# Kernel optimization log

Measured on AMD Instinct MI355X. Metric: run time of the kernel, lower is better.

## Reference

```python
import jax, jax.numpy as jnp
import numpy as np

D = 16        # d_model
DFF = 128     # ffn hidden
H_NN = 128    # pairwise-MLP hidden
RES = 1.0     # res_ratio (undefined global in source; standard residual)
EPS = 1e-6


def setup_inputs() -> dict:
    key = jax.random.key(0)
    ks = jax.random.split(key, 16)
    B, G, L = 8, 1, 256
    def n(k, shape, s=0.05):
        return jax.random.normal(k, shape, jnp.float32) * s
    return dict(
        x=jax.random.normal(ks[0], (B, G, L, D), jnp.float32),
        mask=jnp.zeros((B, G, L, L), jnp.float32),
        wq=n(ks[1], (D, D)), bq=jnp.zeros((D,), jnp.float32),
        wk=n(ks[2], (D, D)), bk=jnp.zeros((D,), jnp.float32),
        wv=n(ks[3], (D, D)), bv=jnp.zeros((D,), jnp.float32),
        wo=n(ks[4], (D, D)), bo=jnp.zeros((D,), jnp.float32),
        nn_w1=n(ks[5], (2 * D, H_NN)), nn_b1=jnp.zeros((H_NN,), jnp.float32),
        nn_w2=n(ks[6], (H_NN, 1)), nn_b2=jnp.zeros((1,), jnp.float32),
        f1=n(ks[7], (D, DFF)), f1b=jnp.zeros((DFF,), jnp.float32),
        f2=n(ks[8], (DFF, D)), f2b=jnp.zeros((D,), jnp.float32),
        g1=jnp.ones((D,), jnp.float32), be1=jnp.zeros((D,), jnp.float32),
        g2=jnp.ones((D,), jnp.float32), be2=jnp.zeros((D,), jnp.float32),
    )


def _layernorm(x, g, b):
    m = jnp.mean(x, -1, keepdims=True)
    v = jnp.var(x, -1, keepdims=True)
    return (x - m) * jax.lax.rsqrt(v + EPS) * g + b


def reference(x, mask, wq, bq, wk, bk, wv, bv, wo, bo,
              nn_w1, nn_b1, nn_w2, nn_b2,
              f1, f1b, f2, f2b, g1, be1, g2, be2):
    # projections: (B,G,L,D)
    q = x @ wq + bq
    k = x @ wk + bk
    v = x @ wv + bv
    # pairwise relation-network attention.
    # NN(concat([q_i, k_j])) first layer splits as q_i @ W1[:D] + k_j @ W1[D:]
    w1q, w1k = nn_w1[:D], nn_w1[D:]
    w2 = nn_w2[:, 0]
    qa = q @ w1q  # (B,G,L,H)
    kb = k @ w1k
    h1 = jax.nn.relu(qa[:, :, :, None, :] + kb[:, :, None, :, :] + nn_b1)  # (B,G,Lq,Lk,H)
    logits = jnp.einsum('bgijh,h->bgij', h1, w2) + nn_b2[0]
    # make_sym: NN(concat([k_j, q_i])) -> k_j @ W1[:D] + q_i @ W1[D:]
    ka = k @ w1q
    qb = q @ w1k
    h2 = jax.nn.relu(qb[:, :, :, None, :] + ka[:, :, None, :, :] + nn_b1)
    logits = logits + jnp.einsum('bgijh,h->bgij', h2, w2) + nn_b2[0]
    logits = logits + mask * -1e9
    attn = jax.nn.softmax(logits, axis=-1)          # (B,G,Lq,Lk)
    ctx = jnp.einsum('bgij,bgjd->bgid', attn, v)    # (B,G,L,D)
    attn_out = ctx @ wo + bo
    out1 = _layernorm(RES * x + (2.0 - RES) * attn_out, g1, be1)
    ffn = jax.nn.relu(out1 @ f1 + f1b) @ f2 + f2b
    out2 = _layernorm(RES * out1 + (2.0 - RES) * ffn, g2, be2)
    return out2
```

## Files before the change

### kernel.cpp

```cpp
#include <hip/hip_runtime.h>
#include <hip/hip_bf16.h>

typedef __hip_bfloat16 bf16;
typedef float f32x4 __attribute__((ext_vector_type(4)));

constexpr int DIM  = 16;
constexpr int HNN  = 128;
constexpr int SEQ  = 256;
constexpr int BAT  = 8;
constexpr int ROWS = BAT * SEQ;
constexpr int HP   = HNN / 2;
constexpr int QT   = 4;
constexpr int NQT  = ROWS / QT;
constexpr int QHP  = 16;

__device__ __forceinline__ bool is_f32(const void* g1) {
  return ((const unsigned*)g1)[0] == 0x3F800000u;
}
__device__ __forceinline__ float ld(const void* p, long i, bool f32) {
  return f32 ? ((const float*)p)[i]
             : __bfloat162float(((const bf16*)p)[i]);
}

__global__ __launch_bounds__(128) void prep_kernel(
    const void* __restrict__ x,
    const void* __restrict__ wq, const void* __restrict__ bq,
    const void* __restrict__ wk, const void* __restrict__ bk,
    const void* __restrict__ wv, const void* __restrict__ bv,
    const void* __restrict__ nn_w1, const void* __restrict__ nn_b1,
    const void* __restrict__ nn_w2, const void* __restrict__ g1flag,
    float* __restrict__ kkT, float* __restrict__ qq,
    float* __restrict__ vT,  float2* __restrict__ w2p)
{
  const bool f32 = is_f32(g1flag);
  const int row = blockIdx.x;
  const int tid = threadIdx.x;
  __shared__ float xs[DIM], qs[DIM], ks[DIM], vs[DIM];

  if (tid < DIM) xs[tid] = ld(x, (long)row * DIM + tid, f32);
  __syncthreads();

  if (tid < 3 * DIM) {
    const int which = tid >> 4, d = tid & 15;
    const void* w  = (which == 0) ? wq : (which == 1) ? wk : wv;
    const void* bb = (which == 0) ? bq : (which == 1) ? bk : bv;
    float acc = ld(bb, d, f32);
    #pragma unroll
    for (int e = 0; e < DIM; e++) acc += xs[e] * ld(w, e * DIM + d, f32);
    if (which == 0) qs[d] = acc;
    else if (which == 1) ks[d] = acc;
    else vs[d] = acc;
  }
  __syncthreads();

  float qw1q = 0.f, qw1k = 0.f, kw1q = 0.f, kw1k = 0.f;
  #pragma unroll
  for (int d = 0; d < DIM; d++) {
    float a = ld(nn_w1, d * HNN + tid, f32);
    float b = ld(nn_w1, (DIM + d) * HNN + tid, f32);
    qw1q += qs[d] * a;  qw1k += qs[d] * b;
    kw1q += ks[d] * a;  kw1k += ks[d] * b;
  }
  const float b1 = ld(nn_b1, tid, f32);
  const int hp = tid >> 1, half = tid & 1;
  ((float2*)kkT)[((size_t)hp * ROWS + row) * 2 + half] =
      make_float2(kw1k + b1, kw1q + b1);
  ((float2*)qq)[((size_t)row * HP + hp) * 2 + half] =
      make_float2(qw1q, qw1k);
  if (tid < DIM) vT[tid * ROWS + row] = vs[tid];
  if (row == 0 && tid < HP)
    w2p[tid] = make_float2(ld(nn_w2, 2 * tid, f32), ld(nn_w2, 2 * tid + 1, f32));
}

__global__ __launch_bounds__(256) void logits_kernel(
    const f32x4* __restrict__ kkT, const f32x4* __restrict__ qq,
    const float2* __restrict__ w2p, float* __restrict__ part)
{
  const int bid     = blockIdx.x;
  const int qt      = bid & (NQT - 1);
  const int quarter = bid >> 9;
  const int bi = qt >> 6;
  const int i0 = (qt & 63) * QT;
  const int j  = threadIdx.x;
  const int col = bi * SEQ + j;

  const f32x4* kkbase = kkT + (size_t)quarter * QHP * ROWS + col;
  const f32x4* qbase  = qq + (size_t)(bi * SEQ + i0) * HP + quarter * QHP;
  const float2* wbase = w2p + quarter * QHP;

  const f32x4 z = {0.f, 0.f, 0.f, 0.f};
  f32x4 acc0 = z, acc1 = z, acc2 = z, acc3 = z;

  #pragma unroll 4
  for (int m = 0; m < QHP; ++m) {
    const f32x4 kk = kkbase[(size_t)m * ROWS];
    const float2 w = wbase[m];
    const f32x4 w4 = {w.x, w.x, w.y, w.y};
    const f32x4 q0 = qbase[0 * HP + m];
    const f32x4 q1 = qbase[1 * HP + m];
    const f32x4 q2 = qbase[2 * HP + m];
    const f32x4 q3 = qbase[3 * HP + m];
    acc0 = __builtin_elementwise_fma(__builtin_elementwise_max(q0 + kk, z), w4, acc0);
    acc1 = __builtin_elementwise_fma(__builtin_elementwise_max(q1 + kk, z), w4, acc1);
    acc2 = __builtin_elementwise_fma(__builtin_elementwise_max(q2 + kk, z), w4, acc2);
    acc3 = __builtin_elementwise_fma(__builtin_elementwise_max(q3 + kk, z), w4, acc3);
  }

  float* dst = part + ((size_t)quarter * ROWS + (bi * SEQ + i0)) * SEQ + j;
  dst[0 * SEQ] = acc0.x + acc0.y + acc0.z + acc0.w;
  dst[1 * SEQ] = acc1.x + acc1.y + acc1.z + acc1.w;
  dst[2 * SEQ] = acc2.x + acc2.y + acc2.z + acc2.w;
  dst[3 * SEQ] = acc3.x + acc3.y + acc3.z + acc3.w;
}

__global__ __launch_bounds__(256) void tail_kernel(
    const void* __restrict__ x,  const void* __restrict__ mask,
    const void* __restrict__ wo, const void* __restrict__ bo,
    const void* __restrict__ nn_b2,
    const void* __restrict__ f1, const void* __restrict__ f1b,
    const void* __restrict__ f2, const void* __restrict__ f2b,
    const void* __restrict__ g1, const void* __restrict__ be1,
    const void* __restrict__ g2, const void* __restrict__ be2,
    const float* __restrict__ part, const float* __restrict__ vT,
    void* __restrict__ out)
{
  const bool f32 = is_f32(g1);
  const int qidx = blockIdx.x;
  const int bi   = qidx >> 8;
  const int j    = threadIdx.x;
  const int col  = bi * SEQ + j;
  const int lane = j & 63, wvi = j >> 6;

  __shared__ float pb[SEQ];
  __shared__ float vbuf[SEQ][DIM + 1];
  __shared__ float red[2][4];
  __shared__ float cpart[DIM][17];
  __shared__ float ctxs[DIM], rr[DIM], o1[DIM], hid[HNN];

  #pragma unroll
  for (int d = 0; d < DIM; ++d) vbuf[j][d] = vT[d * ROWS + col];

  const float* pp = part + (size_t)qidx * SEQ + j;
  const size_t QS = (size_t)ROWS * SEQ;
  float logit = pp[0] + pp[QS] + pp[2 * QS] + pp[3 * QS]
              + 2.f * ld(nn_b2, 0, f32)
              + ld(mask, (size_t)qidx * SEQ + j, f32) * -1e9f;

  float m = logit;
  #pragma unroll
  for (int off = 32; off > 0; off >>= 1) m = fmaxf(m, __shfl_xor(m, off, 64));
  if (lane == 0) red[0][wvi] = m;
  __syncthreads();
  const float mx = fmaxf(fmaxf(red[0][0], red[0][1]), fmaxf(red[0][2], red[0][3]));
  const float e = __expf(logit - mx);
  pb[j] = e;
  float s = e;
  #pragma unroll
  for (int off = 32; off > 0; off >>= 1) s += __shfl_xor(s, off, 64);
  if (lane == 0) red[1][wvi] = s;
  __syncthreads();
  const float inv = 1.f / (red[1][0] + red[1][1] + red[1][2] + red[1][3]);

  {
    const int d = j & 15, c = j >> 4;
    float sacc = 0.f;
    #pragma unroll
    for (int jj = 0; jj < 16; ++jj)
      sacc += pb[c * 16 + jj] * vbuf[c * 16 + jj][d];
    cpart[d][c] = sacc;
  }
  __syncthreads();
  if (j < DIM) {
    float sc = 0.f;
    #pragma unroll
    for (int c = 0; c < 16; ++c) sc += cpart[j][c];
    ctxs[j] = sc * inv;
  }
  __syncthreads();

  if (j < DIM) {
    float ao = ld(bo, j, f32);
    #pragma unroll
    for (int dd = 0; dd < DIM; ++dd) ao += ctxs[dd] * ld(wo, dd * DIM + j, f32);
    rr[j] = ld(x, (long)qidx * DIM + j, f32) + ao;
  }
  __syncthreads();
  if (j < DIM) {
    float mn = 0.f;
    #pragma unroll
    for (int dd = 0; dd < DIM; ++dd) mn += rr[dd];
    mn *= (1.f / DIM);
    float vv = 0.f;
    #pragma unroll
    for (int dd = 0; dd < DIM; ++dd) { float zz = rr[dd] - mn; vv += zz * zz; }
    vv *= (1.f / DIM);
    o1[j] = (rr[j] - mn) * rsqrtf(vv + 1e-6f) * ld(g1, j, f32) + ld(be1, j, f32);
  }
  __syncthreads();

  if (j < HNN) {
    float a = ld(f1b, j, f32);
    #pragma unroll
    for (int dd = 0; dd < DIM; ++dd) a += o1[dd] * ld(f1, dd * HNN + j, f32);
    hid[j] = fmaxf(a, 0.f);
  }
  __syncthreads();

  {
    const int d = j & 15, c = j >> 4;
    float a = 0.f;
    #pragma unroll
    for (int hh = 0; hh < 8; ++hh) {
      const int h = c * 8 + hh;
      a += hid[h] * ld(f2, h * DIM + d, f32);
    }
    cpart[d][c] = a;
  }
  __syncthreads();
  if (j < DIM) {
    float a = ld(f2b, j, f32);
    #pragma unroll
    for (int c = 0; c < 16; ++c) a += cpart[j][c];
    rr[j] = o1[j] + a;
  }
  __syncthreads();

  if (j < DIM) {
    float mn = 0.f;
    #pragma unroll
    for (int dd = 0; dd < DIM; ++dd) mn += rr[dd];
    mn *= (1.f / DIM);
    float vv = 0.f;
    #pragma unroll
    for (int dd = 0; dd < DIM; ++dd) { float zz = rr[dd] - mn; vv += zz * zz; }
    vv *= (1.f / DIM);
    const float val = (rr[j] - mn) * rsqrtf(vv + 1e-6f) * ld(g2, j, f32)
                    + ld(be2, j, f32);
    const long oidx = (long)qidx * DIM + j;
    if (f32) ((float*)out)[oidx] = val;
    else     ((bf16*)out)[oidx] = __float2bfloat16(val);
  }
}

extern "C" void kernel_launch(void* const* d_in, const int* in_sizes, int n_in,
                              void* d_out, int out_size, void* d_ws, size_t ws_size,
                              hipStream_t stream) {
  const void* x     = d_in[0];
  const void* mask  = d_in[1];
  const void* wq    = d_in[2];
  const void* bq    = d_in[3];
  const void* wk    = d_in[4];
  const void* bk    = d_in[5];
  const void* wv    = d_in[6];
  const void* bv    = d_in[7];
  const void* wo    = d_in[8];
  const void* bo    = d_in[9];
  const void* nn_w1 = d_in[10];
  const void* nn_b1 = d_in[11];
  const void* nn_w2 = d_in[12];
  const void* nn_b2 = d_in[13];
  const void* f1    = d_in[14];
  const void* f1b   = d_in[15];
  const void* f2    = d_in[16];
  const void* f2b   = d_in[17];
  const void* g1    = d_in[18];
  const void* be1   = d_in[19];
  const void* g2    = d_in[20];
  const void* be2   = d_in[21];

  float*  kkT  = (float*)d_ws;
  float*  qq   = kkT + (size_t)HP * ROWS * 4;
  float*  vT   = qq  + (size_t)ROWS * HP * 4;
  float*  part = vT  + (size_t)DIM * ROWS;
  float2* w2p  = (float2*)(part + (size_t)4 * ROWS * SEQ);

  prep_kernel<<<ROWS, 128, 0, stream>>>(x, wq, bq, wk, bk, wv, bv,
                                        nn_w1, nn_b1, nn_w2, g1,
                                        kkT, qq, vT, w2p);
  logits_kernel<<<4 * NQT, 256, 0, stream>>>((const f32x4*)kkT, (const f32x4*)qq,
                                             (const float2*)w2p, part);
  tail_kernel<<<ROWS, 256, 0, stream>>>(x, mask, wo, bo, nn_b2,
                                        f1, f1b, f2, f2b, g1, be1, g2, be2,
                                        part, vT, d_out);
}
```

Before: 123.8 us.

## Fuse pairwise logits computation into softmax/FFN tail kernel, four queries per block

Merges the logits kernel and the tail kernel into one kernel where each block handles four query rows over the full hidden dimension. The softmax, context, output projection, layernorms and FFN are done in-block for all four rows. This removes the 4-way split partial-logit buffer and its global write/read round trip plus one launch. In exchange the grid drops from 2048 to 512 blocks, each with a longer serial loop over 64 hidden pairs, which reduces parallelism.

```diff
diff --git a/kernel.cpp b/kernel.cpp
--- a/kernel.cpp
+++ b/kernel.cpp
@@ -12,7 +12,6 @@
 constexpr int HP   = HNN / 2;
 constexpr int QT   = 4;
 constexpr int NQT  = ROWS / QT;
-constexpr int QHP  = 16;
 
 __device__ __forceinline__ bool is_f32(const void* g1) {
   return ((const unsigned*)g1)[0] == 0x3F800000u;
@@ -72,48 +71,7 @@
     w2p[tid] = make_float2(ld(nn_w2, 2 * tid, f32), ld(nn_w2, 2 * tid + 1, f32));
 }
 
-__global__ __launch_bounds__(256) void logits_kernel(
-    const f32x4* __restrict__ kkT, const f32x4* __restrict__ qq,
-    const float2* __restrict__ w2p, float* __restrict__ part)
-{
-  const int bid     = blockIdx.x;
-  const int qt      = bid & (NQT - 1);
-  const int quarter = bid >> 9;
-  const int bi = qt >> 6;
-  const int i0 = (qt & 63) * QT;
-  const int j  = threadIdx.x;
-  const int col = bi * SEQ + j;
-
-  const f32x4* kkbase = kkT + (size_t)quarter * QHP * ROWS + col;
-  const f32x4* qbase  = qq + (size_t)(bi * SEQ + i0) * HP + quarter * QHP;
-  const float2* wbase = w2p + quarter * QHP;
-
-  const f32x4 z = {0.f, 0.f, 0.f, 0.f};
-  f32x4 acc0 = z, acc1 = z, acc2 = z, acc3 = z;
-
-  #pragma unroll 4
-  for (int m = 0; m < QHP; ++m) {
-    const f32x4 kk = kkbase[(size_t)m * ROWS];
-    const float2 w = wbase[m];
-    const f32x4 w4 = {w.x, w.x, w.y, w.y};
-    const f32x4 q0 = qbase[0 * HP + m];
-    const f32x4 q1 = qbase[1 * HP + m];
-    const f32x4 q2 = qbase[2 * HP + m];
-    const f32x4 q3 = qbase[3 * HP + m];
-    acc0 = __builtin_elementwise_fma(__builtin_elementwise_max(q0 + kk, z), w4, acc0);
-    acc1 = __builtin_elementwise_fma(__builtin_elementwise_max(q1 + kk, z), w4, acc1);
-    acc2 = __builtin_elementwise_fma(__builtin_elementwise_max(q2 + kk, z), w4, acc2);
-    acc3 = __builtin_elementwise_fma(__builtin_elementwise_max(q3 + kk, z), w4, acc3);
-  }
-
-  float* dst = part + ((size_t)quarter * ROWS + (bi * SEQ + i0)) * SEQ + j;
-  dst[0 * SEQ] = acc0.x + acc0.y + acc0.z + acc0.w;
-  dst[1 * SEQ] = acc1.x + acc1.y + acc1.z + acc1.w;
-  dst[2 * SEQ] = acc2.x + acc2.y + acc2.z + acc2.w;
-  dst[3 * SEQ] = acc3.x + acc3.y + acc3.z + acc3.w;
-}
-
-__global__ __launch_bounds__(256) void tail_kernel(
+__global__ __launch_bounds__(256) void fused_kernel(
     const void* __restrict__ x,  const void* __restrict__ mask,
     const void* __restrict__ wo, const void* __restrict__ bo,
     const void* __restrict__ nn_b2,
@@ -121,122 +79,179 @@
     const void* __restrict__ f2, const void* __restrict__ f2b,
     const void* __restrict__ g1, const void* __restrict__ be1,
     const void* __restrict__ g2, const void* __restrict__ be2,
-    const float* __restrict__ part, const float* __restrict__ vT,
+    const f32x4* __restrict__ kkT, const f32x4* __restrict__ qq,
+    const float2* __restrict__ w2p, const float* __restrict__ vT,
     void* __restrict__ out)
 {
   const bool f32 = is_f32(g1);
-  const int qidx = blockIdx.x;
-  const int bi   = qidx >> 8;
+  const int qt   = blockIdx.x;
+  const int bi   = qt >> 6;
+  const int i0   = (qt & 63) * QT;
+  const int row0 = bi * SEQ + i0;
   const int j    = threadIdx.x;
   const int col  = bi * SEQ + j;
-  const int lane = j & 63, wvi = j >> 6;
-
-  __shared__ float pb[SEQ];
+  const int lane = j & 63, wv = j >> 6;
+
+  __shared__ float pb[QT][SEQ];
   __shared__ float vbuf[SEQ][DIM + 1];
-  __shared__ float red[2][4];
-  __shared__ float cpart[DIM][17];
-  __shared__ float ctxs[DIM], rr[DIM], o1[DIM], hid[HNN];
+  __shared__ float cpart[QT][DIM][17];
+  __shared__ float mxs[QT], sums[QT];
+  __shared__ float ctxs[QT][DIM], o1s[QT][DIM], rrs[QT][DIM];
+  __shared__ float hid[QT][HNN];
 
   #pragma unroll
   for (int d = 0; d < DIM; ++d) vbuf[j][d] = vT[d * ROWS + col];
 
-  const float* pp = part + (size_t)qidx * SEQ + j;
-  const size_t QS = (size_t)ROWS * SEQ;
-  float logit = pp[0] + pp[QS] + pp[2 * QS] + pp[3 * QS]
-              + 2.f * ld(nn_b2, 0, f32)
-              + ld(mask, (size_t)qidx * SEQ + j, f32) * -1e9f;
-
-  float m = logit;
-  #pragma unroll
-  for (int off = 32; off > 0; off >>= 1) m = fmaxf(m, __shfl_xor(m, off, 64));
-  if (lane == 0) red[0][wvi] = m;
-  __syncthreads();
-  const float mx = fmaxf(fmaxf(red[0][0], red[0][1]), fmaxf(red[0][2], red[0][3]));
-  const float e = __expf(logit - mx);
-  pb[j] = e;
-  float s = e;
-  #pragma unroll
-  for (int off = 32; off > 0; off >>= 1) s += __shfl_xor(s, off, 64);
-  if (lane == 0) red[1][wvi] = s;
-  __syncthreads();
-  const float inv = 1.f / (red[1][0] + red[1][1] + red[1][2] + red[1][3]);
+  const f32x4* kkbase = kkT + col;
+  const f32x4* q0b = qq + (size_t)(row0 + 0) * HP;
+  const f32x4* q1b = qq + (size_t)(row0 + 1) * HP;
+  const f32x4* q2b = qq + (size_t)(row0 + 2) * HP;
+  const f32x4* q3b = qq + (size_t)(row0 + 3) * HP;
+
+  const f32x4 z = {0.f, 0.f, 0.f, 0.f};
+  f32x4 a0 = z, a1 = z, a2 = z, a3 = z;
+
+  #pragma unroll 4
+  for (int m = 0; m < HP; ++m) {
+    const f32x4 kk = kkbase[(size_t)m * ROWS];
+    const float2 w = w2p[m];
+    const f32x4 w4 = {w.x, w.x, w.y, w.y};
+    const f32x4 q0 = q0b[m];
+    const f32x4 q1 = q1b[m];
+    const f32x4 q2 = q2b[m];
+    const f32x4 q3 = q3b[m];
+    a0 = __builtin_elementwise_fma(__builtin_elementwise_max(q0 + kk, z), w4, a0);
+    a1 = __builtin_elementwise_fma(__builtin_elementwise_max(q1 + kk, z), w4, a1);
+    a2 = __builtin_elementwise_fma(__builtin_elementwise_max(q2 + kk, z), w4, a2);
+    a3 = __builtin_elementwise_fma(__builtin_elementwise_max(q3 + kk, z), w4, a3);
+  }
+
+  const float b2 = 2.f * ld(nn_b2, 0, f32);
+  float l0 = a0.x + a0.y + a0.z + a0.w + b2
+           + ld(mask, (size_t)(row0 + 0) * SEQ + j, f32) * -1e9f;
+  float l1 = a1.x + a1.y + a1.z + a1.w + b2
+           + ld(mask, (size_t)(row0 + 1) * SEQ + j, f32) * -1e9f;
+  float l2 = a2.x + a2.y + a2.z + a2.w + b2
+           + ld(mask, (size_t)(row0 + 2) * SEQ + j, f32) * -1e9f;
+  float l3 = a3.x + a3.y + a3.z + a3.w + b2
+           + ld(mask, (size_t)(row0 + 3) * SEQ + j, f32) * -1e9f;
+
+  pb[0][j] = l0; pb[1][j] = l1; pb[2][j] = l2; pb[3][j] = l3;
+  __syncthreads();
+
+  {
+    float m4 = fmaxf(fmaxf(pb[wv][lane],       pb[wv][lane + 64]),
+                     fmaxf(pb[wv][lane + 128], pb[wv][lane + 192]));
+    #pragma unroll
+    for (int off = 32; off > 0; off >>= 1) m4 = fmaxf(m4, __shfl_xor(m4, off, 64));
+    if (lane == 0) mxs[wv] = m4;
+  }
+  __syncthreads();
+  pb[0][j] = __expf(l0 - mxs[0]);
+  pb[1][j] = __expf(l1 - mxs[1]);
+  pb[2][j] = __expf(l2 - mxs[2]);
+  pb[3][j] = __expf(l3 - mxs[3]);
+  __syncthreads();
+  {
+    float s4 = pb[wv][lane] + pb[wv][lane + 64]
+             + pb[wv][lane + 128] + pb[wv][lane + 192];
+    #pragma unroll
+    for (int off = 32; off > 0; off >>= 1) s4 += __shfl_xor(s4, off, 64);
+    if (lane == 0) sums[wv] = s4;
+  }
+  __syncthreads();
 
   {
     const int d = j & 15, c = j >> 4;
-    float sacc = 0.f;
-    #pragma unroll
-    for (int jj = 0; jj < 16; ++jj)
-      sacc += pb[c * 16 + jj] * vbuf[c * 16 + jj][d];
-    cpart[d][c] = sacc;
-  }
-  __syncthreads();
-  if (j < DIM) {
-    float sc = 0.f;
-    #pragma unroll
-    for (int c = 0; c < 16; ++c) sc += cpart[j][c];
-    ctxs[j] = sc * inv;
-  }
-  __syncthreads();
-
-  if (j < DIM) {
-    float ao = ld(bo, j, f32);
-    #pragma unroll
-    for (int dd = 0; dd < DIM; ++dd) ao += ctxs[dd] * ld(wo, dd * DIM + j, f32);
-    rr[j] = ld(x, (long)qidx * DIM + j, f32) + ao;
-  }
-  __syncthreads();
-  if (j < DIM) {
+    #pragma unroll
+    for (int i = 0; i < QT; ++i) {
+      float s = 0.f;
+      #pragma unroll
+      for (int jj = 0; jj < 16; ++jj)
+        s += pb[i][c * 16 + jj] * vbuf[c * 16 + jj][d];
+      cpart[i][d][c] = s;
+    }
+  }
+  __syncthreads();
+  if (j < QT * DIM) {
+    const int i = j >> 4, d = j & 15;
+    float s = 0.f;
+    #pragma unroll
+    for (int c = 0; c < 16; ++c) s += cpart[i][d][c];
+    ctxs[i][d] = s / sums[i];
+  }
+  __syncthreads();
+
+  if (j < QT * DIM) {
+    const int i = j >> 4, d = j & 15;
+    float ao = ld(bo, d, f32);
+    #pragma unroll
+    for (int dd = 0; dd < DIM; ++dd) ao += ctxs[i][dd] * ld(wo, dd * DIM + d, f32);
+    rrs[i][d] = ld(x, (long)(row0 + i) * DIM + d, f32) + ao;
+  }
+  __syncthreads();
+  if (j < QT * DIM) {
+    const int i = j >> 4, d = j & 15;
     float mn = 0.f;
     #pragma unroll
-    for (int dd = 0; dd < DIM; ++dd) mn += rr[dd];
+    for (int dd = 0; dd < DIM; ++dd) mn += rrs[i][dd];
     mn *= (1.f / DIM);
     float vv = 0.f;
     #pragma unroll
-    for (int dd = 0; dd < DIM; ++dd) { float zz = rr[dd] - mn; vv += zz * zz; }
+    for (int dd = 0; dd < DIM; ++dd) { float zz = rrs[i][dd] - mn; vv += zz * zz; }
     vv *= (1.f / DIM);
-    o1[j] = (rr[j] - mn) * rsqrtf(vv + 1e-6f) * ld(g1, j, f32) + ld(be1, j, f32);
-  }
-  __syncthreads();
-
-  if (j < HNN) {
-    float a = ld(f1b, j, f32);
-    #pragma unroll
-    for (int dd = 0; dd < DIM; ++dd) a += o1[dd] * ld(f1, dd * HNN + j, f32);
-    hid[j] = fmaxf(a, 0.f);
+    o1s[i][d] = (rrs[i][d] - mn) * rsqrtf(vv + 1e-6f) * ld(g1, d, f32)
+              + ld(be1, d, f32);
+  }
+  __syncthreads();
+
+  #pragma unroll
+  for (int r = 0; r < 2; ++r) {
+    const int u = r * 256 + j;
+    const int i = u >> 7, h = u & 127;
+    float a = ld(f1b, h, f32);
+    #pragma unroll
+    for (int dd = 0; dd < DIM; ++dd) a += o1s[i][dd] * ld(f1, dd * HNN + h, f32);
+    hid[i][h] = fmaxf(a, 0.f);
   }
   __syncthreads();
 
   {
     const int d = j & 15, c = j >> 4;
-    float a = 0.f;
-    #pragma unroll
-    for (int hh = 0; hh < 8; ++hh) {
-      const int h = c * 8 + hh;
-      a += hid[h] * ld(f2, h * DIM + d, f32);
+    #pragma unroll
+    for (int i = 0; i < QT; ++i) {
+      float a = 0.f;
+      #pragma unroll
+      for (int hh = 0; hh < 8; ++hh) {
+        const int h = c * 8 + hh;
+        a += hid[i][h] * ld(f2, h * DIM + d, f32);
+      }
+      cpart[i][d][c] = a;
     }
-    cpart[d][c] = a;
-  }
-  __syncthreads();
-  if (j < DIM) {
-    float a = ld(f2b, j, f32);
-    #pragma unroll
-    for (int c = 0; c < 16; ++c) a += cpart[j][c];
-    rr[j] = o1[j] + a;
-  }
-  __syncthreads();
-
-  if (j < DIM) {
+  }
+  __syncthreads();
+  if (j < QT * DIM) {
+    const int i = j >> 4, d = j & 15;
+    float a = ld(f2b, d, f32);
+    #pragma unroll
+    for (int c = 0; c < 16; ++c) a += cpart[i][d][c];
+    rrs[i][d] = o1s[i][d] + a;
+  }
+  __syncthreads();
+
+  if (j < QT * DIM) {
+    const int i = j >> 4, d = j & 15;
     float mn = 0.f;
     #pragma unroll
-    for (int dd = 0; dd < DIM; ++dd) mn += rr[dd];
+    for (int dd = 0; dd < DIM; ++dd) mn += rrs[i][dd];
     mn *= (1.f / DIM);
     float vv = 0.f;
     #pragma unroll
-    for (int dd = 0; dd < DIM; ++dd) { float zz = rr[dd] - mn; vv += zz * zz; }
+    for (int dd = 0; dd < DIM; ++dd) { float zz = rrs[i][dd] - mn; vv += zz * zz; }
     vv *= (1.f / DIM);
-    const float val = (rr[j] - mn) * rsqrtf(vv + 1e-6f) * ld(g2, j, f32)
-                    + ld(be2, j, f32);
-    const long oidx = (long)qidx * DIM + j;
+    const float val = (rrs[i][d] - mn) * rsqrtf(vv + 1e-6f) * ld(g2, d, f32)
+                    + ld(be2, d, f32);
+    const long oidx = (long)(row0 + i) * DIM + d;
     if (f32) ((float*)out)[oidx] = val;
     else     ((bf16*)out)[oidx] = __float2bfloat16(val);
   }
@@ -268,18 +283,16 @@
   const void* g2    = d_in[20];
   const void* be2   = d_in[21];
 
-  float*  kkT  = (float*)d_ws;
-  float*  qq   = kkT + (size_t)HP * ROWS * 4;
-  float*  vT   = qq  + (size_t)ROWS * HP * 4;
-  float*  part = vT  + (size_t)DIM * ROWS;
-  float2* w2p  = (float2*)(part + (size_t)4 * ROWS * SEQ);
+  float*  kkT = (float*)d_ws;
+  float*  qq  = kkT + (size_t)HP * ROWS * 4;
+  float*  vT  = qq  + (size_t)ROWS * HP * 4;
+  float2* w2p = (float2*)(vT + (size_t)DIM * ROWS);
 
   prep_kernel<<<ROWS, 128, 0, stream>>>(x, wq, bq, wk, bk, wv, bv,
                                         nn_w1, nn_b1, nn_w2, g1,
                                         kkT, qq, vT, w2p);
-  logits_kernel<<<4 * NQT, 256, 0, stream>>>((const f32x4*)kkT, (const f32x4*)qq,
-                                             (const float2*)w2p, part);
-  tail_kernel<<<ROWS, 256, 0, stream>>>(x, mask, wo, bo, nn_b2,
+  fused_kernel<<<NQT, 256, 0, stream>>>(x, mask, wo, bo, nn_b2,
                                         f1, f1b, f2, f2b, g1, be1, g2, be2,
-                                        part, vT, d_out);
-}
+                                        (const f32x4*)kkT, (const f32x4*)qq,
+                                        (const float2*)w2p, vT, d_out);
+}
```

After: 122.3 us. About the same (-1.2%).
